# Kernel optimization log

Measured on AMD Instinct MI355X. Metric: run time of the kernel, lower is better.

The kernel has to match this reference:

```python
import jax, jax.numpy as jnp
import numpy as np

TEMP = 0.07
LAMBDA_CON = 1.0
LAMBDA_SHELL = 1.0
NEG_INF = -1e30


def setup_inputs() -> dict:
    key = jax.random.key(0)
    k1, k2, k3, k4, k5 = jax.random.split(key, 5)
    B, D = 8192, 1024
    emb = jax.random.normal(k1, (B, D), jnp.float32)
    emb = emb / jnp.linalg.norm(emb, axis=1, keepdims=True)  # encoder outputs are unit-norm
    center = jax.random.normal(k2, (D,), jnp.float32)
    center = center / jnp.linalg.norm(center)  # buffer is F.normalize'd in estimate_epoch_geometry
    labels = jax.random.randint(k3, (B,), 0, 2)  # 0 = machine, 1 = human
    radius_m = jax.random.uniform(k4, (1,), jnp.float32)
    radius_h = radius_m + jax.random.uniform(k5, (1,), jnp.float32)  # radius_h >= radius_m by construction
    return {"embeddings": emb, "center": center, "radius_m": radius_m,
            "radius_h": radius_h, "labels": labels}


def reference(embeddings, center, radius_m, radius_h, labels):
    rm = radius_m[0]
    rh = radius_h[0]
    B = embeddings.shape[0]

    # ---- shell loss ----
    distances = jnp.linalg.norm(embeddings - center[None, :], axis=1)  # [B]
    mmask = labels == 0
    hmask = labels == 1
    nm = jnp.sum(mmask)
    nh = jnp.sum(hmask)
    loss_m = jnp.sum(jnp.where(mmask, jnp.square(jax.nn.relu(distances - rm)), 0.0)) / jnp.maximum(nm, 1)
    loss_h = jnp.sum(jnp.where(hmask, jnp.square(jax.nn.relu(rh - distances)), 0.0)) / jnp.maximum(nh, 1)
    loss_shell = loss_m + loss_h

    # ---- contrastive loss (batched: one BxB sim matrix instead of per-anchor loop) ----
    S = (embeddings @ embeddings.T) / TEMP          # [B, B] pairwise logits
    Sp = (embeddings @ center) / TEMP               # [B]  logits vs prototype
    eye = jnp.eye(B, dtype=bool)
    S_masked = jnp.where(eye, jnp.asarray(NEG_INF, S.dtype), S)
    # denominator per machine anchor i: logsumexp over {other machines, prototype, humans}
    # (labels are only 0/1, so all j != i contribute) plus the prototype logit
    lse = jnp.logaddexp(jax.nn.logsumexp(S_masked, axis=1), Sp)  # [B]
    # positives for machine anchor i: other machines (nm-1) + prototype -> nm positives
    pos_sum = jnp.sum(jnp.where(mmask[None, :] & ~eye, S, 0.0), axis=1) + Sp  # [B]
    anchor_loss = lse - pos_sum / jnp.maximum(nm, 1)
    con_sum = jnp.sum(jnp.where(mmask, anchor_loss, 0.0))
    # prototype as anchor: positives = machines, negatives = humans
    lse_p = jax.nn.logsumexp(Sp)
    proto_loss = lse_p - jnp.sum(jnp.where(mmask, Sp, 0.0)) / jnp.maximum(nm, 1)
    loss_con = (con_sum + proto_loss) / jnp.maximum(nm + 1, 1)
    # original returns 0 when either class is empty
    both = (nm > 0) & (nh > 0)
    loss_con = jnp.where(both, loss_con, 0.0)

    loss = LAMBDA_SHELL * loss_shell + LAMBDA_CON * loss_con
    return (loss, loss_shell, loss_m, loss_h, loss_con, distances)
```

## Files before the change

### kernel.cpp

```cpp
#include <hip/hip_runtime.h>

#define INV_T 14.285714285714286f
#define C1 0.055803571428571425f

typedef float f32x16 __attribute__((ext_vector_type(16)));
typedef float f32x4 __attribute__((ext_vector_type(4)));
typedef int i32x4v __attribute__((ext_vector_type(4)));
typedef int i32x8 __attribute__((ext_vector_type(8)));

__device__ __forceinline__ unsigned char f2e4m3(float f) {
    unsigned char s = (unsigned char)((__float_as_uint(f) >> 24) & 0x80);
    float a = fabsf(f);
    if (a > 448.f) a = 448.f;
    if (a == 0.f) return s;
    int e = (int)((__float_as_uint(a) >> 23) & 0xFF) - 127;
    if (e < -10) return s;
    if (e < -6) e = -6;
    float scale = __int_as_float((unsigned)(130 - e) << 23);
    int mi = (int)rintf(a * scale);
    if (mi >= 16) { mi >>= 1; ++e; }
    if (mi < 8) return s | (unsigned char)mi;
    return s | (unsigned char)(((e + 7) << 3) | (mi - 8));
}

__device__ __forceinline__ void async16(void* l, const void* g) {
    __builtin_amdgcn_global_load_lds(
        (const __attribute__((address_space(1))) unsigned int*)g,
        (__attribute__((address_space(3))) unsigned int*)l, 16, 0, 0);
}

__global__ void __launch_bounds__(256) k_prep(const float* __restrict__ emb,
                                              const float* __restrict__ center,
                                              unsigned char* __restrict__ embQ,
                                              float* __restrict__ out,
                                              float* __restrict__ Sp, int D, int B) {
    int tid = threadIdx.x;
    int wave = tid >> 6, lane = tid & 63;
    int gw = blockIdx.x * 4 + wave;
    int nw = gridDim.x * 4;
    const float4* c4 = (const float4*)center;
    for (int i = gw; i < B; i += nw) {
        const float4* row = (const float4*)(emb + (size_t)i * D);
        uchar4* qrow = embQ ? (uchar4*)(embQ + (size_t)i * D) : nullptr;
        float d2 = 0.f, sp = 0.f;
#pragma unroll
        for (int j = 0; j < 4; ++j) {
            int idx = lane + j * 64;
            float4 e = row[idx];
            float4 c = c4[idx];
            float dx = e.x - c.x, dy = e.y - c.y, dz = e.z - c.z, dw = e.w - c.w;
            d2 += dx * dx + dy * dy + dz * dz + dw * dw;
            sp += e.x * c.x + e.y * c.y + e.z * c.z + e.w * c.w;
            if (qrow)
                qrow[idx] = make_uchar4(f2e4m3(e.x * 16.f), f2e4m3(e.y * 16.f),
                                        f2e4m3(e.z * 16.f), f2e4m3(e.w * 16.f));
        }
#pragma unroll
        for (int m = 1; m <= 32; m <<= 1) {
            d2 += __shfl_xor(d2, m, 64);
            sp += __shfl_xor(sp, m, 64);
        }
        if (lane == 0) {
            out[5 + i] = sqrtf(d2);
            Sp[i] = sp * INV_T;
        }
    }
}

__global__ void __launch_bounds__(256) k_colsum(const float* __restrict__ emb,
                                                const int* __restrict__ labels,
                                                float* __restrict__ s_m,
                                                int* __restrict__ cnt, int D) {
    int t = threadIdx.x;
    int r0 = blockIdx.x * 32;
    float4 acc = {0.f, 0.f, 0.f, 0.f};
#pragma unroll 4
    for (int r = 0; r < 32; ++r) {
        float sc = (labels[r0 + r] == 0) ? 1.f : 0.f;
        float4 v = ((const float4*)(emb + (size_t)(r0 + r) * D))[t];
        acc.x += v.x * sc; acc.y += v.y * sc; acc.z += v.z * sc; acc.w += v.w * sc;
    }
    atomicAdd(&s_m[t * 4 + 0], acc.x);
    atomicAdd(&s_m[t * 4 + 1], acc.y);
    atomicAdd(&s_m[t * 4 + 2], acc.z);
    atomicAdd(&s_m[t * 4 + 3], acc.w);
    if (t == 0) {
        int c = 0;
        for (int r = 0; r < 32; ++r) c += (labels[r0 + r] == 0) ? 1 : 0;
        atomicAdd(cnt, c);
    }
}

#define MXMFMA(a, b, c) __builtin_amdgcn_mfma_scale_f32_32x32x64_f8f6f4( \
    (a), (b), (c), 0, 0, 0, 0x7F7F7F7F, 0, 0x7F7F7F7F)

__global__ void __launch_bounds__(256, 2)
k_sumexp_mx(const unsigned char* __restrict__ embQ, float* __restrict__ sumexp,
            int D, int nT) {
    int bid = blockIdx.x;
    const int n = nT;
    float nf = (float)n + 0.5f;
    int rb = (int)(nf - sqrtf(fmaxf(nf * nf - 2.0f * (float)bid, 0.f)));
    if (rb < 0) rb = 0;
    if (rb > n - 1) rb = n - 1;
#define TRI_OFF(r) ((r) * n - ((r) * ((r)-1)) / 2)
    while (rb + 1 <= n - 1 && TRI_OFF(rb + 1) <= bid) ++rb;
    while (rb > 0 && TRI_OFF(rb) > bid) --rb;
    int cb = rb + (bid - TRI_OFF(rb));
#undef TRI_OFF
    int rowbase = rb * 128, colbase = cb * 128;

    int tid = threadIdx.x;
    int wave = tid >> 6, lane = tid & 63;
    int wr = wave >> 1, wc = wave & 1;
    int l31 = lane & 31, kk = lane >> 5;

    __shared__ unsigned char sA[2][16384];
    __shared__ unsigned char sB[2][16384];
    __shared__ float rred[2][128];
    __shared__ float cred[2][128];

    f32x16 acc[2][2];
#pragma unroll
    for (int fr = 0; fr < 2; ++fr)
#pragma unroll
        for (int fc = 0; fc < 2; ++fc)
#pragma unroll
            for (int v = 0; v < 16; ++v) acc[fr][fc][v] = 0.f;

    const int kG = D >> 7;

    const unsigned char* gSA[4];
    const unsigned char* gSB[4];
    unsigned int dstOff[4];
#pragma unroll
    for (int q = 0; q < 4; ++q) {
        int ch = q * 256 + tid;
        int row = ch >> 3, lc = ch & 7;
        int gc = lc ^ (row & 7);
        gSA[q] = embQ + (size_t)(rowbase + row) * D + gc * 16;
        gSB[q] = embQ + (size_t)(colbase + row) * D + gc * 16;
        dstOff[q] = (unsigned)ch << 4;
    }

    auto stage = [&](int buf, int kt) {
        int ko = kt << 7;
#pragma unroll
        for (int q = 0; q < 4; ++q) {
            async16(&sA[buf][dstOff[q]], gSA[q] + ko);
            async16(&sB[buf][dstOff[q]], gSB[q] + ko);
        }
    };

    int e7 = (l31 & 7) << 4;
    int offs[2][2];
#pragma unroll
    for (int h = 0; h < 2; ++h)
#pragma unroll
        for (int j = 0; j < 2; ++j)
            offs[h][j] = (((h * 4 + kk * 2 + j) << 4) ^ e7);
    int aBase0 = (wr * 64 + l31) << 7;
    int aBase1 = aBase0 + (32 << 7);
    int bBase0 = (wc * 64 + l31) << 7;
    int bBase1 = bBase0 + (32 << 7);

    stage(0, 0);
    for (int kt = 0; kt < kG; ++kt) {
        int cur = kt & 1;
        __syncthreads();
        if (kt + 1 < kG) stage(cur ^ 1, kt + 1);
        const unsigned char* A = sA[cur];
        const unsigned char* Bp = sB[cur];
#pragma unroll
        for (int h = 0; h < 2; ++h) {
            i32x8 av[2], bv[2];
            {
                i32x4v lo = *(const i32x4v*)&A[aBase0 + offs[h][0]];
                i32x4v hi = *(const i32x4v*)&A[aBase0 + offs[h][1]];
                av[0] = __builtin_shufflevector(lo, hi, 0, 1, 2, 3, 4, 5, 6, 7);
            }
            {
                i32x4v lo = *(const i32x4v*)&A[aBase1 + offs[h][0]];
                i32x4v hi = *(const i32x4v*)&A[aBase1 + offs[h][1]];
                av[1] = __builtin_shufflevector(lo, hi, 0, 1, 2, 3, 4, 5, 6, 7);
            }
            {
                i32x4v lo = *(const i32x4v*)&Bp[bBase0 + offs[h][0]];
                i32x4v hi = *(const i32x4v*)&Bp[bBase0 + offs[h][1]];
                bv[0] = __builtin_shufflevector(lo, hi, 0, 1, 2, 3, 4, 5, 6, 7);
            }
            {
                i32x4v lo = *(const i32x4v*)&Bp[bBase1 + offs[h][0]];
                i32x4v hi = *(const i32x4v*)&Bp[bBase1 + offs[h][1]];
                bv[1] = __builtin_shufflevector(lo, hi, 0, 1, 2, 3, 4, 5, 6, 7);
            }
#pragma unroll
            for (int fr = 0; fr < 2; ++fr)
#pragma unroll
                for (int fc = 0; fc < 2; ++fc)
                    acc[fr][fc] = MXMFMA(av[fr], bv[fc], acc[fr][fc]);
        }
    }

    float rs[2][16];
    float cs[2] = {0.f, 0.f};
#pragma unroll
    for (int fr = 0; fr < 2; ++fr)
#pragma unroll
        for (int v = 0; v < 16; ++v) rs[fr][v] = 0.f;

#pragma unroll
    for (int fr = 0; fr < 2; ++fr)
#pragma unroll
        for (int fc = 0; fc < 2; ++fc) {
            int gcol = colbase + wc * 64 + fc * 32 + l31;
#pragma unroll
            for (int v = 0; v < 16; ++v) {
                int grow = rowbase + wr * 64 + fr * 32 + (v & 3) + 8 * (v >> 2) + 4 * kk;
                float e = (grow < gcol) ? __expf(acc[fr][fc][v] * C1 - INV_T) : 0.f;
                rs[fr][v] += e;
                cs[fc] += e;
            }
        }

#pragma unroll
    for (int m = 1; m <= 16; m <<= 1)
#pragma unroll
        for (int fr = 0; fr < 2; ++fr)
#pragma unroll
            for (int v = 0; v < 16; ++v) rs[fr][v] += __shfl_xor(rs[fr][v], m, 64);
    if (l31 == 0)
#pragma unroll
        for (int fr = 0; fr < 2; ++fr)
#pragma unroll
            for (int v = 0; v < 16; ++v)
                rred[wc][wr * 64 + fr * 32 + (v & 3) + 8 * (v >> 2) + 4 * kk] = rs[fr][v];

#pragma unroll
    for (int fc = 0; fc < 2; ++fc) cs[fc] += __shfl_xor(cs[fc], 32, 64);
    if (kk == 0)
#pragma unroll
        for (int fc = 0; fc < 2; ++fc) cred[wr][wc * 64 + fc * 32 + l31] = cs[fc];

    __syncthreads();
    if (tid < 128) {
        atomicAdd(&sumexp[rowbase + tid], rred[0][tid] + rred[1][tid]);
    } else {
        int u = tid - 128;
        atomicAdd(&sumexp[colbase + u], cred[0][u] + cred[1][u]);
    }
}

typedef __bf16 bf16x8 __attribute__((ext_vector_type(8)));
typedef unsigned short u16x8 __attribute__((ext_vector_type(8)));
__device__ __forceinline__ unsigned short f2bf(float f) {
    unsigned int x = __float_as_uint(f);
    x += 0x7fffu + ((x >> 16) & 1u);
    return (unsigned short)(x >> 16);
}
__global__ void __launch_bounds__(256) k_sumexp_fb(const float* __restrict__ embF,
                                                   float* __restrict__ sumexp, int D, int nTiles) {
    int bid = blockIdx.x;
    const int n = nTiles;
    float nf = (float)n + 0.5f;
    int rb = (int)(nf - sqrtf(fmaxf(nf * nf - 2.0f * (float)bid, 0.f)));
    if (rb < 0) rb = 0;
    if (rb > n - 1) rb = n - 1;
#define TRI_OFF(r) ((r) * n - ((r) * ((r)-1)) / 2)
    while (rb + 1 <= n - 1 && TRI_OFF(rb + 1) <= bid) ++rb;
    while (rb > 0 && TRI_OFF(rb) > bid) --rb;
    int cb = rb + (bid - TRI_OFF(rb));
#undef TRI_OFF
    int tid = threadIdx.x;
    int wave = tid >> 6, lane = tid & 63;
    int wr = wave >> 1, wc = wave & 1;
    int quad = lane >> 4, l15 = lane & 15;
    int rowbase = rb * 128, colbase = cb * 128;
    __shared__ unsigned short lA[128 * 64];
    __shared__ unsigned short lB[128 * 64];
    __shared__ float rred[2][128];
    __shared__ float cred[2][128];
    f32x4 zero = {0.f, 0.f, 0.f, 0.f};
    f32x4 acc[4][4];
#pragma unroll
    for (int r = 0; r < 4; ++r)
#pragma unroll
        for (int c = 0; c < 4; ++c) acc[r][c] = zero;
    const int kIters = D >> 6;
    for (int kt = 0; kt < kIters; ++kt) {
        int k0 = kt << 6;
#pragma unroll
        for (int q = 0; q < 4; ++q) {
            int ch = q * 256 + tid;
            int row = ch >> 3, lc = ch & 7;
            int pc = lc ^ (row & 7);
            const float4* sa = (const float4*)(embF + (size_t)(rowbase + row) * D + k0 + lc * 8);
            const float4* sb = (const float4*)(embF + (size_t)(colbase + row) * D + k0 + lc * 8);
            float4 a0 = sa[0], a1 = sa[1];
            float4 b0 = sb[0], b1 = sb[1];
            u16x8 va = {f2bf(a0.x), f2bf(a0.y), f2bf(a0.z), f2bf(a0.w),
                        f2bf(a1.x), f2bf(a1.y), f2bf(a1.z), f2bf(a1.w)};
            u16x8 vb = {f2bf(b0.x), f2bf(b0.y), f2bf(b0.z), f2bf(b0.w),
                        f2bf(b1.x), f2bf(b1.y), f2bf(b1.z), f2bf(b1.w)};
            *(u16x8*)&lA[(row << 6) + (pc << 3)] = va;
            *(u16x8*)&lB[(row << 6) + (pc << 3)] = vb;
        }
        __syncthreads();
#pragma unroll
        for (int h = 0; h < 2; ++h) {
            bf16x8 af[4], bfr[4];
#pragma unroll
            for (int r = 0; r < 4; ++r) {
                int row = wr * 64 + r * 16 + l15;
                int pc = (h * 4 + quad) ^ (l15 & 7);
                af[r] = *(const bf16x8*)&lA[(row << 6) + (pc << 3)];
            }
#pragma unroll
            for (int c = 0; c < 4; ++c) {
                int row = wc * 64 + c * 16 + l15;
                int pc = (h * 4 + quad) ^ (l15 & 7);
                bfr[c] = *(const bf16x8*)&lB[(row << 6) + (pc << 3)];
            }
#pragma unroll
            for (int r = 0; r < 4; ++r)
#pragma unroll
                for (int c = 0; c < 4; ++c)
                    acc[r][c] = __builtin_amdgcn_mfma_f32_16x16x32_bf16(af[r], bfr[c], acc[r][c], 0, 0, 0);
        }
        __syncthreads();
    }
    float rs[4][4], cs[4];
#pragma unroll
    for (int r = 0; r < 4; ++r)
#pragma unroll
        for (int v = 0; v < 4; ++v) rs[r][v] = 0.f;
#pragma unroll
    for (int c = 0; c < 4; ++c) cs[c] = 0.f;
#pragma unroll
    for (int r = 0; r < 4; ++r)
#pragma unroll
        for (int c = 0; c < 4; ++c) {
            f32x4 a = acc[r][c];
            int gcol = colbase + wc * 64 + c * 16 + l15;
#pragma unroll
            for (int v = 0; v < 4; ++v) {
                int grow = rowbase + wr * 64 + r * 16 + quad * 4 + v;
                float e = (grow < gcol) ? __expf((a[v] - 1.0f) * INV_T) : 0.f;
                rs[r][v] += e;
                cs[c] += e;
            }
        }
#pragma unroll
    for (int m = 1; m <= 8; m <<= 1)
#pragma unroll
        for (int r = 0; r < 4; ++r)
#pragma unroll
            for (int v = 0; v < 4; ++v) rs[r][v] += __shfl_xor(rs[r][v], m, 64);
    if (l15 == 0)
#pragma unroll
        for (int r = 0; r < 4; ++r)
#pragma unroll
            for (int v = 0; v < 4; ++v)
                rred[wc][wr * 64 + r * 16 + quad * 4 + v] = rs[r][v];
#pragma unroll
    for (int m = 16; m <= 32; m <<= 1)
#pragma unroll
        for (int c = 0; c < 4; ++c) cs[c] += __shfl_xor(cs[c], m, 64);
    if (quad == 0)
#pragma unroll
        for (int c = 0; c < 4; ++c) cred[wr][wc * 64 + c * 16 + l15] = cs[c];
    __syncthreads();
    if (tid < 128) {
        atomicAdd(&sumexp[rowbase + tid], rred[0][tid] + rred[1][tid]);
    } else {
        int u = tid & 127;
        atomicAdd(&sumexp[colbase + u], cred[0][u] + cred[1][u]);
    }
}

__global__ void __launch_bounds__(256) k_finalize(const float* __restrict__ emb,
                                                  const float* __restrict__ s_m,
                                                  const float* __restrict__ Sp,
                                                  const float* __restrict__ sumexp,
                                                  const int* __restrict__ labels,
                                                  const float* __restrict__ outv,
                                                  const float* __restrict__ rmp,
                                                  const float* __restrict__ rhp,
                                                  float* __restrict__ scal, int D) {
    int tid = threadIdx.x;
    int wave = tid >> 6, lane = tid & 63;
    __shared__ float ac[8];
    if (tid < 8) ac[tid] = 0.f;
    __syncthreads();
    float rm = rmp[0], rh = rhp[0];
    const float4* sm4 = (const float4*)s_m;
    for (int it = 0; it < 8; ++it) {
        int i = blockIdx.x * 32 + it * 4 + wave;
        const float4* row = (const float4*)(emb + (size_t)i * D);
        float q = 0.f, sd = 0.f;
#pragma unroll
        for (int j = 0; j < 4; ++j) {
            int idx = lane + j * 64;
            float4 e = row[idx];
            float4 s = sm4[idx];
            q += e.x * s.x + e.y * s.y + e.z * s.z + e.w * s.w;
            sd += e.x * e.x + e.y * e.y + e.z * e.z + e.w * e.w;
        }
#pragma unroll
        for (int m = 1; m <= 32; m <<= 1) {
            q += __shfl_xor(q, m, 64);
            sd += __shfl_xor(sd, m, 64);
        }
        if (lane == 0) {
            float LP = Sp[i];
            float eS = __expf(LP - INV_T);
            float lse = INV_T + __logf(sumexp[i] + eS);
            bool mach = (labels[i] == 0);
            float pos = (q - (mach ? sd : 0.f)) * INV_T + LP;
            float d = outv[5 + i];
            atomicAdd(&ac[2], eS);
            if (mach) {
                atomicAdd(&ac[4], lse);
                atomicAdd(&ac[5], pos);
                atomicAdd(&ac[3], LP);
                float x = d - rm;
                if (x > 0.f) atomicAdd(&ac[0], x * x);
            } else {
                float x = rh - d;
                if (x > 0.f) atomicAdd(&ac[1], x * x);
            }
        }
    }
    __syncthreads();
    if (tid < 8) atomicAdd(&scal[tid], ac[tid]);
}

__global__ void k_final(const float* __restrict__ scal, const int* __restrict__ cnt,
                        float* __restrict__ out, int B) {
    if (threadIdx.x == 0) {
        int nm = cnt[0], nh = B - nm;
        float nmf = (float)(nm > 1 ? nm : 1);
        float nhf = (float)(nh > 1 ? nh : 1);
        float loss_m = scal[0] / nmf;
        float loss_h = scal[1] / nhf;
        float loss_shell = loss_m + loss_h;
        float lse_p = INV_T + __logf(scal[2]);
        float proto = lse_p - scal[3] / nmf;
        float con = scal[4] - scal[5] / nmf;
        int denom = (nm + 1 > 1) ? nm + 1 : 1;
        float lc = (con + proto) / (float)denom;
        if (!(nm > 0 && nh > 0)) lc = 0.f;
        out[0] = loss_shell + lc;
        out[1] = loss_shell;
        out[2] = loss_m;
        out[3] = loss_h;
        out[4] = lc;
    }
}

extern "C" void kernel_launch(void* const* d_in, const int* in_sizes, int n_in,
                              void* d_out, int out_size, void* d_ws, size_t ws_size,
                              hipStream_t stream) {
    const float* emb = (const float*)d_in[0];
    const float* center = (const float*)d_in[1];
    const float* rmp = (const float*)d_in[2];
    const float* rhp = (const float*)d_in[3];
    const int* labels = (const int*)d_in[4];
    float* out = (float*)d_out;
    const int B = in_sizes[4];
    const int D = in_sizes[1];

    size_t qBytes = (size_t)B * D;
    size_t auxBytes = (size_t)B * 4 + (size_t)D * 4 + 256 + (size_t)B * 4;
    bool pre = ws_size >= qBytes + auxBytes;
    size_t Z0 = pre ? qBytes : 0;

    char* ws = (char*)d_ws;
    unsigned char* embQ = (unsigned char*)ws;
    float* sumexp = (float*)(ws + Z0);
    float* s_m = (float*)(ws + Z0 + (size_t)B * 4);
    float* scal = (float*)(ws + Z0 + (size_t)B * 4 + (size_t)D * 4);
    int* cnt = (int*)(scal + 8);
    float* Sp = (float*)(ws + Z0 + (size_t)B * 4 + (size_t)D * 4 + 256);

    hipMemsetAsync(ws + Z0, 0, (size_t)B * 4 + (size_t)D * 4 + 256, stream);

    k_prep<<<512, 256, 0, stream>>>(emb, center, pre ? embQ : nullptr, out, Sp, D, B);
    k_colsum<<<B / 32, D / 4, 0, stream>>>(emb, labels, s_m, cnt, D);

    int nT = B / 128;
    int nBlocks = nT * (nT + 1) / 2;
    if (pre) k_sumexp_mx<<<nBlocks, 256, 0, stream>>>(embQ, sumexp, D, nT);
    else     k_sumexp_fb<<<nBlocks, 256, 0, stream>>>(emb, sumexp, D, nT);

    k_finalize<<<B / 32, 256, 0, stream>>>(emb, s_m, Sp, sumexp, labels, out, rmp, rhp, scal, D);
    k_final<<<1, 64, 0, stream>>>(scal, cnt, out, B);
}
```

Before: 200.7 us.

## Fuse column-sum into prep kernel and halve MX GEMM K-tile for occupancy

Folds the labelled column-sum (s_m, machine count) into k_prep, so emb is read once instead of twice and one launch is removed. The per-wave partial sums are reduced through LDS before the atomics. Separately, the FP8 MFMA sumexp kernel now stages a 64-byte K slice per step instead of 128, halving its LDS footprint, and raises launch_bounds occupancy from 2 to 4 blocks. The cost is twice as many K-loop iterations and barriers, with less MFMA work between each sync.

Result: slower. 208.1 us (+3.7%).

```diff
diff --git a/kernel.cpp b/kernel.cpp
--- a/kernel.cpp
+++ b/kernel.cpp
@@ -31,26 +31,39 @@
 
 __global__ void __launch_bounds__(256) k_prep(const float* __restrict__ emb,
                                               const float* __restrict__ center,
+                                              const int* __restrict__ labels,
                                               unsigned char* __restrict__ embQ,
                                               float* __restrict__ out,
-                                              float* __restrict__ Sp, int D, int B) {
+                                              float* __restrict__ Sp,
+                                              float* __restrict__ s_m,
+                                              int* __restrict__ cnt, int D) {
     int tid = threadIdx.x;
     int wave = tid >> 6, lane = tid & 63;
-    int gw = blockIdx.x * 4 + wave;
-    int nw = gridDim.x * 4;
+    int r0 = blockIdx.x * 32;
+    __shared__ float ldsCS[4][1024];
     const float4* c4 = (const float4*)center;
-    for (int i = gw; i < B; i += nw) {
+    float4 c[4];
+#pragma unroll
+    for (int j = 0; j < 4; ++j) c[j] = c4[lane + j * 64];
+    float4 acc[4];
+#pragma unroll
+    for (int j = 0; j < 4; ++j) acc[j] = make_float4(0.f, 0.f, 0.f, 0.f);
+
+    for (int k = 0; k < 8; ++k) {
+        int i = r0 + wave * 8 + k;
         const float4* row = (const float4*)(emb + (size_t)i * D);
         uchar4* qrow = embQ ? (uchar4*)(embQ + (size_t)i * D) : nullptr;
+        float lb = (labels[i] == 0) ? 1.f : 0.f;
         float d2 = 0.f, sp = 0.f;
 #pragma unroll
         for (int j = 0; j < 4; ++j) {
             int idx = lane + j * 64;
             float4 e = row[idx];
-            float4 c = c4[idx];
-            float dx = e.x - c.x, dy = e.y - c.y, dz = e.z - c.z, dw = e.w - c.w;
+            float dx = e.x - c[j].x, dy = e.y - c[j].y, dz = e.z - c[j].z, dw = e.w - c[j].w;
             d2 += dx * dx + dy * dy + dz * dz + dw * dw;
-            sp += e.x * c.x + e.y * c.y + e.z * c.z + e.w * c.w;
+            sp += e.x * c[j].x + e.y * c[j].y + e.z * c[j].z + e.w * c[j].w;
+            acc[j].x += e.x * lb; acc[j].y += e.y * lb;
+            acc[j].z += e.z * lb; acc[j].w += e.w * lb;
             if (qrow)
                 qrow[idx] = make_uchar4(f2e4m3(e.x * 16.f), f2e4m3(e.y * 16.f),
                                         f2e4m3(e.z * 16.f), f2e4m3(e.w * 16.f));
@@ -65,36 +78,29 @@
             Sp[i] = sp * INV_T;
         }
     }
-}
-
-__global__ void __launch_bounds__(256) k_colsum(const float* __restrict__ emb,
-                                                const int* __restrict__ labels,
-                                                float* __restrict__ s_m,
-                                                int* __restrict__ cnt, int D) {
-    int t = threadIdx.x;
-    int r0 = blockIdx.x * 32;
-    float4 acc = {0.f, 0.f, 0.f, 0.f};
-#pragma unroll 4
-    for (int r = 0; r < 32; ++r) {
-        float sc = (labels[r0 + r] == 0) ? 1.f : 0.f;
-        float4 v = ((const float4*)(emb + (size_t)(r0 + r) * D))[t];
-        acc.x += v.x * sc; acc.y += v.y * sc; acc.z += v.z * sc; acc.w += v.w * sc;
-    }
-    atomicAdd(&s_m[t * 4 + 0], acc.x);
-    atomicAdd(&s_m[t * 4 + 1], acc.y);
-    atomicAdd(&s_m[t * 4 + 2], acc.z);
-    atomicAdd(&s_m[t * 4 + 3], acc.w);
-    if (t == 0) {
-        int c = 0;
-        for (int r = 0; r < 32; ++r) c += (labels[r0 + r] == 0) ? 1 : 0;
-        atomicAdd(cnt, c);
+#pragma unroll
+    for (int j = 0; j < 4; ++j)
+        *(float4*)&ldsCS[wave][4 * (lane + j * 64)] = acc[j];
+    __syncthreads();
+    float4 s0 = *(float4*)&ldsCS[0][tid * 4];
+    float4 s1 = *(float4*)&ldsCS[1][tid * 4];
+    float4 s2 = *(float4*)&ldsCS[2][tid * 4];
+    float4 s3 = *(float4*)&ldsCS[3][tid * 4];
+    atomicAdd(&s_m[tid * 4 + 0], s0.x + s1.x + s2.x + s3.x);
+    atomicAdd(&s_m[tid * 4 + 1], s0.y + s1.y + s2.y + s3.y);
+    atomicAdd(&s_m[tid * 4 + 2], s0.z + s1.z + s2.z + s3.z);
+    atomicAdd(&s_m[tid * 4 + 3], s0.w + s1.w + s2.w + s3.w);
+    if (tid == 0) {
+        int cm = 0;
+        for (int r = 0; r < 32; ++r) cm += (labels[r0 + r] == 0) ? 1 : 0;
+        atomicAdd(cnt, cm);
     }
 }
 
 #define MXMFMA(a, b, c) __builtin_amdgcn_mfma_scale_f32_32x32x64_f8f6f4( \
     (a), (b), (c), 0, 0, 0, 0x7F7F7F7F, 0, 0x7F7F7F7F)
 
-__global__ void __launch_bounds__(256, 2)
+__global__ void __launch_bounds__(256, 4)
 k_sumexp_mx(const unsigned char* __restrict__ embQ, float* __restrict__ sumexp,
             int D, int nT) {
     int bid = blockIdx.x;
@@ -115,8 +121,8 @@
     int wr = wave >> 1, wc = wave & 1;
     int l31 = lane & 31, kk = lane >> 5;
 
-    __shared__ unsigned char sA[2][16384];
-    __shared__ unsigned char sB[2][16384];
+    __shared__ unsigned char sA[2][8192];
+    __shared__ unsigned char sB[2][8192];
     __shared__ float rred[2][128];
     __shared__ float cred[2][128];
 
@@ -128,41 +134,37 @@
 #pragma unroll
             for (int v = 0; v < 16; ++v) acc[fr][fc][v] = 0.f;
 
-    const int kG = D >> 7;
-
-    const unsigned char* gSA[4];
-    const unsigned char* gSB[4];
-    unsigned int dstOff[4];
-#pragma unroll
-    for (int q = 0; q < 4; ++q) {
+    const int kG = D >> 6;
+
+    const unsigned char* gSA[2];
+    const unsigned char* gSB[2];
+    unsigned int dstOff[2];
+#pragma unroll
+    for (int q = 0; q < 2; ++q) {
         int ch = q * 256 + tid;
-        int row = ch >> 3, lc = ch & 7;
-        int gc = lc ^ (row & 7);
+        int row = ch >> 2, lc = ch & 3;
+        int gc = lc ^ (row & 3);
         gSA[q] = embQ + (size_t)(rowbase + row) * D + gc * 16;
         gSB[q] = embQ + (size_t)(colbase + row) * D + gc * 16;
         dstOff[q] = (unsigned)ch << 4;
     }
 
     auto stage = [&](int buf, int kt) {
-        int ko = kt << 7;
-#pragma unroll
-        for (int q = 0; q < 4; ++q) {
+        int ko = kt << 6;
+#pragma unroll
+        for (int q = 0; q < 2; ++q) {
             async16(&sA[buf][dstOff[q]], gSA[q] + ko);
             async16(&sB[buf][dstOff[q]], gSB[q] + ko);
         }
     };
 
-    int e7 = (l31 & 7) << 4;
-    int offs[2][2];
-#pragma unroll
-    for (int h = 0; h < 2; ++h)
-#pragma unroll
-        for (int j = 0; j < 2; ++j)
-            offs[h][j] = (((h * 4 + kk * 2 + j) << 4) ^ e7);
-    int aBase0 = (wr * 64 + l31) << 7;
-    int aBase1 = aBase0 + (32 << 7);
-    int bBase0 = (wc * 64 + l31) << 7;
-    int bBase1 = bBase0 + (32 << 7);
+    int e3 = l31 & 3;
+    int off0 = ((kk * 2 + 0) ^ e3) << 4;
+    int off1 = ((kk * 2 + 1) ^ e3) << 4;
+    int aBase0 = (wr * 64 + l31) << 6;
+    int aBase1 = aBase0 + (32 << 6);
+    int bBase0 = (wc * 64 + l31) << 6;
+    int bBase1 = bBase0 + (32 << 6);
 
     stage(0, 0);
     for (int kt = 0; kt < kG; ++kt) {
@@ -171,35 +173,32 @@
         if (kt + 1 < kG) stage(cur ^ 1, kt + 1);
         const unsigned char* A = sA[cur];
         const unsigned char* Bp = sB[cur];
-#pragma unroll
-        for (int h = 0; h < 2; ++h) {
-            i32x8 av[2], bv[2];
-            {
-                i32x4v lo = *(const i32x4v*)&A[aBase0 + offs[h][0]];
-                i32x4v hi = *(const i32x4v*)&A[aBase0 + offs[h][1]];
-                av[0] = __builtin_shufflevector(lo, hi, 0, 1, 2, 3, 4, 5, 6, 7);
-            }
-            {
-                i32x4v lo = *(const i32x4v*)&A[aBase1 + offs[h][0]];
-                i32x4v hi = *(const i32x4v*)&A[aBase1 + offs[h][1]];
-                av[1] = __builtin_shufflevector(lo, hi, 0, 1, 2, 3, 4, 5, 6, 7);
-            }
-            {
-                i32x4v lo = *(const i32x4v*)&Bp[bBase0 + offs[h][0]];
-                i32x4v hi = *(const i32x4v*)&Bp[bBase0 + offs[h][1]];
-                bv[0] = __builtin_shufflevector(lo, hi, 0, 1, 2, 3, 4, 5, 6, 7);
-            }
-            {
-                i32x4v lo = *(const i32x4v*)&Bp[bBase1 + offs[h][0]];
-                i32x4v hi = *(const i32x4v*)&Bp[bBase1 + offs[h][1]];
-                bv[1] = __builtin_shufflevector(lo, hi, 0, 1, 2, 3, 4, 5, 6, 7);
-            }
-#pragma unroll
-            for (int fr = 0; fr < 2; ++fr)
-#pragma unroll
-                for (int fc = 0; fc < 2; ++fc)
-                    acc[fr][fc] = MXMFMA(av[fr], bv[fc], acc[fr][fc]);
-        }
+        i32x8 av[2], bv[2];
+        {
+            i32x4v lo = *(const i32x4v*)&A[aBase0 + off0];
+            i32x4v hi = *(const i32x4v*)&A[aBase0 + off1];
+            av[0] = __builtin_shufflevector(lo, hi, 0, 1, 2, 3, 4, 5, 6, 7);
+        }
+        {
+            i32x4v lo = *(const i32x4v*)&A[aBase1 + off0];
+            i32x4v hi = *(const i32x4v*)&A[aBase1 + off1];
+            av[1] = __builtin_shufflevector(lo, hi, 0, 1, 2, 3, 4, 5, 6, 7);
+        }
+        {
+            i32x4v lo = *(const i32x4v*)&Bp[bBase0 + off0];
+            i32x4v hi = *(const i32x4v*)&Bp[bBase0 + off1];
+            bv[0] = __builtin_shufflevector(lo, hi, 0, 1, 2, 3, 4, 5, 6, 7);
+        }
+        {
+            i32x4v lo = *(const i32x4v*)&Bp[bBase1 + off0];
+            i32x4v hi = *(const i32x4v*)&Bp[bBase1 + off1];
+            bv[1] = __builtin_shufflevector(lo, hi, 0, 1, 2, 3, 4, 5, 6, 7);
+        }
+#pragma unroll
+        for (int fr = 0; fr < 2; ++fr)
+#pragma unroll
+            for (int fc = 0; fc < 2; ++fc)
+                acc[fr][fc] = MXMFMA(av[fr], bv[fc], acc[fr][fc]);
     }
 
     float rs[2][16];
@@ -485,8 +484,8 @@
 
     hipMemsetAsync(ws + Z0, 0, (size_t)B * 4 + (size_t)D * 4 + 256, stream);
 
-    k_prep<<<512, 256, 0, stream>>>(emb, center, pre ? embQ : nullptr, out, Sp, D, B);
-    k_colsum<<<B / 32, D / 4, 0, stream>>>(emb, labels, s_m, cnt, D);
+    k_prep<<<B / 32, 256, 0, stream>>>(emb, center, labels, pre ? embQ : nullptr,
+                                       out, Sp, s_m, cnt, D);
 
     int nT = B / 128;
     int nBlocks = nT * (nT + 1) / 2;
```
